# Kernel tuning notes

Measured on AMD Instinct MI355X. Metric: run time of the kernel, lower is better.

The kernel has to match this reference:

```python
import jax, jax.numpy as jnp
import numpy as np

EMD_DIM = 64
NB_EMD = 512


def setup_inputs() -> dict:
    key = jax.random.key(0)
    k_x, k_e = jax.random.split(key)
    x = jax.random.normal(k_x, (32, 64, 64, EMD_DIM), dtype=jnp.float32)
    # codebook buffer, shape [emd_dim, nb_emd] as in the torch module
    embed = jax.random.normal(k_e, (EMD_DIM, NB_EMD), dtype=jnp.float32)
    return {"x": x, "embed": embed}


def reference(x, embed):
    # Eval-mode forward (the EMA buffer update only runs under self.training
    # and does not affect this forward's outputs).
    flatten = x.reshape(-1, EMD_DIM)                      # [N, d]
    dist = (jnp.sum(flatten * flatten, axis=1, keepdims=True)
            - 2.0 * flatten @ embed
            + jnp.sum(embed * embed, axis=0, keepdims=True))  # [N, K]
    emd_id_flat = jnp.argmax(-dist, axis=1)               # nearest code index [N]
    emd_id = emd_id_flat.reshape(x.shape[:-1])            # [B, H, W]
    q = jnp.take(embed.T, emd_id, axis=0)                 # gather codes -> [B,H,W,d]
    diff = jnp.mean((jax.lax.stop_gradient(q) - x) ** 2)  # commitment loss
    q_st = x + jax.lax.stop_gradient(q - x)               # straight-through
    return (q_st, diff, emd_id)
```

## Files before the change

kernel.cpp:

```cpp
#include <hip/hip_runtime.h>

#define N_VEC 131072
#define D 64
#define K 512
#define GUARD 0.05f
#define NB_GATHER 2048
#define FB_Q 16

typedef __attribute__((ext_vector_type(8))) short bf16x8;
typedef __attribute__((ext_vector_type(4))) float f32x4;

static __device__ __forceinline__ short f2bf(float f) {
  unsigned u = __builtin_bit_cast(unsigned, f);
  u += 0x7fffu + ((u >> 16) & 1u);
  return (short)(u >> 16);
}
static __device__ __forceinline__ float bf2f(short h) {
  unsigned u = ((unsigned)(unsigned short)h) << 16;
  return __builtin_bit_cast(float, u);
}
static __device__ __forceinline__ void split8(const float4 f0, const float4 f1,
                                              bf16x8& h, bf16x8& m) {
  const float v[8] = {f0.x, f0.y, f0.z, f0.w, f1.x, f1.y, f1.z, f1.w};
#pragma unroll
  for (int j = 0; j < 8; ++j) {
    const short hh = f2bf(v[j]);
    h[j] = hh;
    m[j] = f2bf(v[j] - bf2f(hh));
  }
}

__global__ __launch_bounds__(64) void vq_prep_kernel(
    const float* __restrict__ embed, float* __restrict__ et,
    float* __restrict__ nrm, bf16x8* __restrict__ F, int* __restrict__ cnt)
{
  const int b = blockIdx.x;
  const int lane = threadIdx.x;
  if (b < 32) {
    const int row = lane & 15;
    const int kg  = lane >> 4;
    const int code = b * 16 + row;
#pragma unroll
    for (int c = 0; c < 2; ++c) {
      bf16x8 h, m;
#pragma unroll
      for (int j = 0; j < 8; ++j) {
        const int d = kg * 8 + c * 32 + j;
        const float e = embed[d * K + code];
        const short hh = f2bf(e);
        h[j] = hh;
        m[j] = f2bf(e - bf2f(hh));
      }
      F[b * 256 + c * 128 + 0  + lane] = h;
      F[b * 256 + c * 128 + 64 + lane] = m;
    }
  } else {
    if (b == 32 && lane == 0) cnt[0] = 0;
    const int code = (b - 32) * 64 + lane;
    float s = 0.f;
#pragma unroll
    for (int d = 0; d < D; ++d) {
      const float e = embed[d * K + code];
      et[code * D + d] = e;
      s = fmaf(e, e, s);
    }
    nrm[code] = s;
  }
}

#define MFMA12(P0, Q0, P1, Q1, BH0, BM0, BH1, BM1) do {                        \
    P0 = __builtin_amdgcn_mfma_f32_16x16x32_bf16(Ah0c0, BH0, kZero, 0, 0, 0); \
    P1 = __builtin_amdgcn_mfma_f32_16x16x32_bf16(Ah1c0, BH0, kZero, 0, 0, 0); \
    Q0 = __builtin_amdgcn_mfma_f32_16x16x32_bf16(Ah0c1, BM1, kZero, 0, 0, 0); \
    Q1 = __builtin_amdgcn_mfma_f32_16x16x32_bf16(Ah1c1, BM1, kZero, 0, 0, 0); \
    P0 = __builtin_amdgcn_mfma_f32_16x16x32_bf16(Ah0c1, BH1, P0, 0, 0, 0);    \
    P1 = __builtin_amdgcn_mfma_f32_16x16x32_bf16(Ah1c1, BH1, P1, 0, 0, 0);    \
    Q0 = __builtin_amdgcn_mfma_f32_16x16x32_bf16(Am0c0, BH0, Q0, 0, 0, 0);    \
    Q1 = __builtin_amdgcn_mfma_f32_16x16x32_bf16(Am1c0, BH0, Q1, 0, 0, 0);    \
    P0 = __builtin_amdgcn_mfma_f32_16x16x32_bf16(Ah0c0, BM0, P0, 0, 0, 0);    \
    P1 = __builtin_amdgcn_mfma_f32_16x16x32_bf16(Ah1c0, BM0, P1, 0, 0, 0);    \
    Q0 = __builtin_amdgcn_mfma_f32_16x16x32_bf16(Am0c1, BH1, Q0, 0, 0, 0);    \
    Q1 = __builtin_amdgcn_mfma_f32_16x16x32_bf16(Am1c1, BH1, Q1, 0, 0, 0);    \
  } while (0)

#define SCORE4(P0, Q0, P1, Q1, CODE, NV) do {                                  \
    _Pragma("unroll")                                                          \
    for (int r = 0; r < 4; ++r) {                                              \
      const float s0 = fmaf(-2.f, P0[r], fmaf(-2.f, Q0[r], (NV)));             \
      b2[r] = __builtin_amdgcn_fmed3f(s0, b1[r], b2[r]);                       \
      if (s0 < b1[r]) { b1[r] = s0; i1[r] = (CODE); }                          \
      const float s1 = fmaf(-2.f, P1[r], fmaf(-2.f, Q1[r], (NV)));             \
      b2[4 + r] = __builtin_amdgcn_fmed3f(s1, b1[4 + r], b2[4 + r]);           \
      if (s1 < b1[4 + r]) { b1[4 + r] = s1; i1[4 + r] = (CODE); }              \
    }                                                                          \
  } while (0)

#define LOADB(BH0, BM0, BH1, BM1, PTR) do {                                    \
    BH0 = (PTR)[0]; BM0 = (PTR)[64]; BH1 = (PTR)[128]; BM1 = (PTR)[192];       \
  } while (0)

__global__ __launch_bounds__(64, 3) void vq_coarse_kernel(
    const float* __restrict__ x, const bf16x8* __restrict__ F,
    const float* __restrict__ nrm, float* __restrict__ idf,
    int* __restrict__ cnt, int* __restrict__ list)
{
  const int lane = threadIdx.x;
  const int wid  = blockIdx.x;
  const int qbase = wid * 32;
  const int row = lane & 15;
  const int kg  = lane >> 4;

  bf16x8 Ah0c0, Ah0c1, Ah1c0, Ah1c1, Am0c0, Am0c1, Am1c0, Am1c1;
  {
    const float* xr0 = x + (size_t)(qbase + row) * D + kg * 8;
    const float* xr1 = x + (size_t)(qbase + 16 + row) * D + kg * 8;
    split8(*reinterpret_cast<const float4*>(xr0),
           *reinterpret_cast<const float4*>(xr0 + 4), Ah0c0, Am0c0);
    split8(*reinterpret_cast<const float4*>(xr0 + 32),
           *reinterpret_cast<const float4*>(xr0 + 36), Ah0c1, Am0c1);
    split8(*reinterpret_cast<const float4*>(xr1),
           *reinterpret_cast<const float4*>(xr1 + 4), Ah1c0, Am1c0);
    split8(*reinterpret_cast<const float4*>(xr1 + 32),
           *reinterpret_cast<const float4*>(xr1 + 36), Ah1c1, Am1c1);
  }

  float b1[8], b2[8]; int i1[8];
#pragma unroll
  for (int r = 0; r < 8; ++r) { b1[r] = 3.4e38f; b2[r] = 3.4e38f; i1[r] = 0; }

  const f32x4 kZero = {0.f, 0.f, 0.f, 0.f};
  bf16x8 X0h0, X0m0, X0h1, X0m1;
  bf16x8 X1h0, X1m0, X1h1, X1m1;
  f32x4 pA0, qA0, pA1, qA1;
  f32x4 pB0, qB0, pB1, qB1;

  const bf16x8* fp = F + lane;
  const float* np = nrm + row;

  float nvA  = np[0];
  float nvBc = np[16];
  np += 32;
  LOADB(X0h0, X0m0, X0h1, X0m1, fp);
  LOADB(X1h0, X1m0, X1h1, X1m1, fp + 256);
  fp += 512;
  MFMA12(pA0, qA0, pA1, qA1, X0h0, X0m0, X0h1, X0m1);
  LOADB(X0h0, X0m0, X0h1, X0m1, fp);
  fp += 256;
  MFMA12(pB0, qB0, pB1, qB1, X1h0, X1m0, X1h1, X1m1);
  SCORE4(pA0, qA0, pA1, qA1, row, nvA);

#pragma unroll 1
  for (int tp = 2; tp <= 30; tp += 2) {
    const float nvA2 = np[0];
    const float nvB  = np[16];
    np += 32;
    LOADB(X1h0, X1m0, X1h1, X1m1, fp);
    MFMA12(pA0, qA0, pA1, qA1, X0h0, X0m0, X0h1, X0m1);
    SCORE4(pB0, qB0, pB1, qB1, (tp - 1) * 16 + row, nvBc);
    LOADB(X0h0, X0m0, X0h1, X0m1, fp + 256);
    fp += 512;
    MFMA12(pB0, qB0, pB1, qB1, X1h0, X1m0, X1h1, X1m1);
    SCORE4(pA0, qA0, pA1, qA1, tp * 16 + row, nvA2);
    nvBc = nvB;
  }
  SCORE4(pB0, qB0, pB1, qB1, 31 * 16 + row, nvBc);

#pragma unroll
  for (int m = 1; m < 16; m <<= 1) {
#pragma unroll
    for (int r = 0; r < 8; ++r) {
      const float o1 = __shfl_xor(b1[r], m, 64);
      const int   oi = __shfl_xor(i1[r], m, 64);
      const float o2 = __shfl_xor(b2[r], m, 64);
      if (o1 < b1[r]) { b2[r] = fminf(b1[r], o2); b1[r] = o1; i1[r] = oi; }
      else            { b2[r] = fminf(b2[r], o1); }
    }
  }

  unsigned m32 = 0;
  if (row == 0) {
#pragma unroll
    for (int r = 0; r < 8; ++r) {
      const int qoff = (r >> 2) * 16 + kg * 4 + (r & 3);
      idf[qbase + qoff] = (float)i1[r];
      if (b2[r] - b1[r] < GUARD) m32 |= 1u << qoff;
    }
  }
  m32 |= __shfl_xor((int)m32, 16, 64);
  m32 |= __shfl_xor((int)m32, 32, 64);
  if (lane == 0 && m32) {
    int base = atomicAdd(cnt, __popc(m32));
    while (m32) {
      const int b = __ffs(m32) - 1;
      m32 &= m32 - 1;
      list[base++] = qbase + b;
    }
  }
}

__global__ __launch_bounds__(256) void vq_fallback_kernel(
    const float* __restrict__ x, const float* __restrict__ embed,
    const float* __restrict__ nrm, const int* __restrict__ cnt,
    const int* __restrict__ list, float* __restrict__ idf)
{
  __shared__ float x_lds[FB_Q * D];
  __shared__ int   s_qidx[FB_Q];
  __shared__ float s_best[4][FB_Q];
  __shared__ int   s_bid[4][FB_Q];
  const int tid  = threadIdx.x;
  const int lane = tid & 63;
  const int wv   = tid >> 6;
  const int n = cnt[0];

  for (int qb = blockIdx.x * FB_Q; qb < n; qb += gridDim.x * FB_Q) {
    __syncthreads();
    if (tid < FB_Q) {
      const int idx = qb + tid;
      s_qidx[tid] = list[idx < n ? idx : qb];
    }
    __syncthreads();
    {
      const int qj = tid >> 4, dq = tid & 15;
      *reinterpret_cast<float4*>(&x_lds[qj * D + dq * 4]) =
          *reinterpret_cast<const float4*>(x + (size_t)s_qidx[qj] * D + dq * 4);
    }
    __syncthreads();

    const int c0 = wv * 128 + lane;
    const int c1 = c0 + 64;
    float a0[FB_Q], a1[FB_Q];
#pragma unroll
    for (int i = 0; i < FB_Q; ++i) { a0[i] = 0.f; a1[i] = 0.f; }

#pragma unroll 4
    for (int ch = 0; ch < 16; ++ch) {
      const int d0 = ch * 4;
      const float e00 = embed[(d0 + 0) * K + c0];
      const float e01 = embed[(d0 + 0) * K + c1];
      const float e10 = embed[(d0 + 1) * K + c0];
      const float e11 = embed[(d0 + 1) * K + c1];
      const float e20 = embed[(d0 + 2) * K + c0];
      const float e21 = embed[(d0 + 2) * K + c1];
      const float e30 = embed[(d0 + 3) * K + c0];
      const float e31 = embed[(d0 + 3) * K + c1];
#pragma unroll
      for (int i = 0; i < FB_Q; ++i) {
        const float4 xv = *reinterpret_cast<const float4*>(&x_lds[i * D + d0]);
        a0[i] = fmaf(xv.x, e00, a0[i]);
        a0[i] = fmaf(xv.y, e10, a0[i]);
        a0[i] = fmaf(xv.z, e20, a0[i]);
        a0[i] = fmaf(xv.w, e30, a0[i]);
        a1[i] = fmaf(xv.x, e01, a1[i]);
        a1[i] = fmaf(xv.y, e11, a1[i]);
        a1[i] = fmaf(xv.z, e21, a1[i]);
        a1[i] = fmaf(xv.w, e31, a1[i]);
      }
    }

    const float nr0 = nrm[c0], nr1 = nrm[c1];
#pragma unroll
    for (int i = 0; i < FB_Q; ++i) {
      float best; int bid;
      const float s0 = fmaf(-2.f, a0[i], nr0);
      best = s0; bid = c0;
      const float s1 = fmaf(-2.f, a1[i], nr1);
      if (s1 < best) { best = s1; bid = c1; }
#pragma unroll
      for (int off = 32; off > 0; off >>= 1) {
        const float s2 = __shfl_down(best, off, 64);
        const int   b2 = __shfl_down(bid, off, 64);
        if (s2 < best || (s2 == best && b2 < bid)) { best = s2; bid = b2; }
      }
      if (lane == 0) { s_best[wv][i] = best; s_bid[wv][i] = bid; }
    }
    __syncthreads();
    if (tid < FB_Q) {
      float best = s_best[0][tid]; int bid = s_bid[0][tid];
#pragma unroll
      for (int w = 1; w < 4; ++w) {
        const float s = s_best[w][tid];
        if (s < best) { best = s; bid = s_bid[w][tid]; }
      }
      idf[s_qidx[tid]] = (float)bid;
    }
  }
}

__global__ __launch_bounds__(256) void vq_gather_kernel(
    const float* __restrict__ x, const float* __restrict__ et,
    const float* __restrict__ idf, float* __restrict__ q,
    float* __restrict__ partial)
{
  const int tid = blockIdx.x * 256 + threadIdx.x;
  const int stride = gridDim.x * 256;
  float acc = 0.f;
  for (int idx = tid; idx < N_VEC * (D / 4); idx += stride) {
    const int v = idx >> 4;
    const int d4 = idx & 15;
    const int id = (int)idf[v];
    const float4 xv = reinterpret_cast<const float4*>(x)[idx];
    const float4 ev = reinterpret_cast<const float4*>(et)[(id << 4) + d4];
    const float e0 = ev.x - xv.x, e1 = ev.y - xv.y, e2 = ev.z - xv.z, e3 = ev.w - xv.w;
    acc += (e0 * e0 + e1 * e1) + (e2 * e2 + e3 * e3);
    reinterpret_cast<float4*>(q)[idx] = ev;
  }
  acc += __shfl_down(acc, 32, 64);
  acc += __shfl_down(acc, 16, 64);
  acc += __shfl_down(acc, 8, 64);
  acc += __shfl_down(acc, 4, 64);
  acc += __shfl_down(acc, 2, 64);
  acc += __shfl_down(acc, 1, 64);
  __shared__ float sred[4];
  if ((threadIdx.x & 63) == 0) sred[threadIdx.x >> 6] = acc;
  __syncthreads();
  if (threadIdx.x == 0)
    partial[blockIdx.x] = (sred[0] + sred[1]) + (sred[2] + sred[3]);
}

__global__ __launch_bounds__(256) void vq_finalize_kernel(
    const float* __restrict__ partial, float* __restrict__ out)
{
  float acc = 0.f;
  for (int i = threadIdx.x; i < NB_GATHER; i += 256) acc += partial[i];
  acc += __shfl_down(acc, 32, 64);
  acc += __shfl_down(acc, 16, 64);
  acc += __shfl_down(acc, 8, 64);
  acc += __shfl_down(acc, 4, 64);
  acc += __shfl_down(acc, 2, 64);
  acc += __shfl_down(acc, 1, 64);
  __shared__ float sred[4];
  if ((threadIdx.x & 63) == 0) sred[threadIdx.x >> 6] = acc;
  __syncthreads();
  if (threadIdx.x == 0)
    out[0] = ((sred[0] + sred[1]) + (sred[2] + sred[3])) * (1.0f / (float)(N_VEC * D));
}

extern "C" void kernel_launch(void* const* d_in, const int* in_sizes, int n_in,
                              void* d_out, int out_size, void* d_ws, size_t ws_size,
                              hipStream_t stream) {
  const float* x = (const float*)d_in[0];
  const float* embed = (const float*)d_in[1];
  float* out = (float*)d_out;
  float* q    = out;
  float* diff = out + 8388608;
  float* idf  = out + 8388609;

  float* ws = (float*)d_ws;
  float* et      = ws;
  float* nrm     = ws + 32768;
  float* partial = ws + 33312;
  int*   cnt     = (int*)(ws + 35360);
  int*   list    = (int*)(ws + 35368);
  bf16x8* F = (bf16x8*)(ws + 35368 + N_VEC);

  vq_prep_kernel<<<40, 64, 0, stream>>>(embed, et, nrm, F, cnt);
  vq_coarse_kernel<<<N_VEC / 32, 64, 0, stream>>>(x, F, nrm, idf, cnt, list);
  vq_fallback_kernel<<<1024, 256, 0, stream>>>(x, embed, nrm, cnt, list, idf);
  vq_gather_kernel<<<NB_GATHER, 256, 0, stream>>>(x, et, idf, q, partial);
  vq_finalize_kernel<<<1, 256, 0, stream>>>(partial, diff);
}
```

Before: 83.86 us.

## Fuse gather and loss into coarse kernel, stage codebook hi-part in LDS

The coarse kernel now runs 512-thread blocks that stage the bf16 high part of the codebook in shared memory and stream the low part from global memory. The separate gather and reduction pass is removed. Each wave writes its quantized rows and accumulates the squared error for confident queries directly after the argmin. Fallback queries write their own q rows and a per-query error into a zeroed buffer, which two small kernels reduce. This avoids re-reading x and the indices in a separate gather pass, at the cost of a 64 KB LDS footprint that limits occupancy, an extra memset, and an extra finalize launch.

```diff
diff --git a/kernel.cpp b/kernel.cpp
--- a/kernel.cpp
+++ b/kernel.cpp
@@ -4,7 +4,6 @@
 #define D 64
 #define K 512
 #define GUARD 0.05f
-#define NB_GATHER 2048
 #define FB_Q 16
 
 typedef __attribute__((ext_vector_type(8))) short bf16x8;
@@ -32,7 +31,8 @@
 
 __global__ __launch_bounds__(64) void vq_prep_kernel(
     const float* __restrict__ embed, float* __restrict__ et,
-    float* __restrict__ nrm, bf16x8* __restrict__ F, int* __restrict__ cnt)
+    float* __restrict__ nrm, bf16x8* __restrict__ FH, bf16x8* __restrict__ FM,
+    int* __restrict__ cnt)
 {
   const int b = blockIdx.x;
   const int lane = threadIdx.x;
@@ -51,8 +51,8 @@
         h[j] = hh;
         m[j] = f2bf(e - bf2f(hh));
       }
-      F[b * 256 + c * 128 + 0  + lane] = h;
-      F[b * 256 + c * 128 + 64 + lane] = m;
+      FH[b * 128 + c * 64 + lane] = h;
+      FM[b * 128 + c * 64 + lane] = m;
     }
   } else {
     if (b == 32 && lane == 0) cnt[0] = 0;
@@ -95,20 +95,27 @@
     }                                                                          \
   } while (0)
 
-#define LOADB(BH0, BM0, BH1, BM1, PTR) do {                                    \
-    BH0 = (PTR)[0]; BM0 = (PTR)[64]; BH1 = (PTR)[128]; BM1 = (PTR)[192];       \
-  } while (0)
-
-__global__ __launch_bounds__(64, 3) void vq_coarse_kernel(
-    const float* __restrict__ x, const bf16x8* __restrict__ F,
-    const float* __restrict__ nrm, float* __restrict__ idf,
-    int* __restrict__ cnt, int* __restrict__ list)
+__global__ __launch_bounds__(512, 4) void vq_coarse_kernel(
+    const float* __restrict__ x, const bf16x8* __restrict__ FH,
+    const bf16x8* __restrict__ FM, const float* __restrict__ nrm,
+    const float* __restrict__ et, float* __restrict__ qout,
+    float* __restrict__ idf, int* __restrict__ cnt, int* __restrict__ list,
+    float* __restrict__ cpart)
 {
-  const int lane = threadIdx.x;
-  const int wid  = blockIdx.x;
-  const int qbase = wid * 32;
-  const int row = lane & 15;
-  const int kg  = lane >> 4;
+  __shared__ bf16x8 LBH[4096];
+  const int tid  = threadIdx.x;
+  const int lane = tid & 63;
+  const int w    = tid >> 6;
+  const int row  = lane & 15;
+  const int kg   = lane >> 4;
+  const int qbase = blockIdx.x * 256 + w * 32;
+
+  {
+    const float4* src = reinterpret_cast<const float4*>(FH);
+    float4* dst = reinterpret_cast<float4*>(LBH);
+#pragma unroll
+    for (int j = 0; j < 8; ++j) dst[tid + j * 512] = src[tid + j * 512];
+  }
 
   bf16x8 Ah0c0, Ah0c1, Ah1c0, Ah1c1, Am0c0, Am0c1, Am1c0, Am1c1;
   {
@@ -123,47 +130,35 @@
     split8(*reinterpret_cast<const float4*>(xr1 + 32),
            *reinterpret_cast<const float4*>(xr1 + 36), Ah1c1, Am1c1);
   }
+  __syncthreads();
 
   float b1[8], b2[8]; int i1[8];
 #pragma unroll
   for (int r = 0; r < 8; ++r) { b1[r] = 3.4e38f; b2[r] = 3.4e38f; i1[r] = 0; }
 
   const f32x4 kZero = {0.f, 0.f, 0.f, 0.f};
-  bf16x8 X0h0, X0m0, X0h1, X0m1;
-  bf16x8 X1h0, X1m0, X1h1, X1m1;
-  f32x4 pA0, qA0, pA1, qA1;
-  f32x4 pB0, qB0, pB1, qB1;
-
-  const bf16x8* fp = F + lane;
-  const float* np = nrm + row;
-
-  float nvA  = np[0];
-  float nvBc = np[16];
-  np += 32;
-  LOADB(X0h0, X0m0, X0h1, X0m1, fp);
-  LOADB(X1h0, X1m0, X1h1, X1m1, fp + 256);
-  fp += 512;
-  MFMA12(pA0, qA0, pA1, qA1, X0h0, X0m0, X0h1, X0m1);
-  LOADB(X0h0, X0m0, X0h1, X0m1, fp);
-  fp += 256;
-  MFMA12(pB0, qB0, pB1, qB1, X1h0, X1m0, X1h1, X1m1);
-  SCORE4(pA0, qA0, pA1, qA1, row, nvA);
+  f32x4 aP0, aQ0, aP1, aQ1;
+
+  const bf16x8* fm = FM + lane;
+  const float*  np = nrm + row;
+  const bf16x8* lb = LBH + lane;
+  bf16x8 Bm0 = fm[0], Bm1 = fm[64]; fm += 128;
+  float nv = np[0]; np += 16;
 
 #pragma unroll 1
-  for (int tp = 2; tp <= 30; tp += 2) {
-    const float nvA2 = np[0];
-    const float nvB  = np[16];
-    np += 32;
-    LOADB(X1h0, X1m0, X1h1, X1m1, fp);
-    MFMA12(pA0, qA0, pA1, qA1, X0h0, X0m0, X0h1, X0m1);
-    SCORE4(pB0, qB0, pB1, qB1, (tp - 1) * 16 + row, nvBc);
-    LOADB(X0h0, X0m0, X0h1, X0m1, fp + 256);
-    fp += 512;
-    MFMA12(pB0, qB0, pB1, qB1, X1h0, X1m0, X1h1, X1m1);
-    SCORE4(pA0, qA0, pA1, qA1, tp * 16 + row, nvA2);
-    nvBc = nvB;
-  }
-  SCORE4(pB0, qB0, pB1, qB1, 31 * 16 + row, nvBc);
+  for (int t = 0; t < 32; ++t) {
+    const bf16x8 Bh0 = lb[0];
+    const bf16x8 Bh1 = lb[64];
+    lb += 128;
+    const bf16x8 nBm0 = fm[0];
+    const bf16x8 nBm1 = fm[64];
+    fm += 128;
+    const float nnv = np[0];
+    np += 16;
+    MFMA12(aP0, aQ0, aP1, aQ1, Bh0, Bm0, Bh1, Bm1);
+    SCORE4(aP0, aQ0, aP1, aQ1, t * 16 + row, nv);
+    Bm0 = nBm0; Bm1 = nBm1; nv = nnv;
+  }
 
 #pragma unroll
   for (int m = 1; m < 16; m <<= 1) {
@@ -196,17 +191,54 @@
       list[base++] = qbase + b;
     }
   }
+
+  float wacc = 0.f;
+  const float* xw = x + (size_t)qbase * D;
+  float* qw = qout + (size_t)qbase * D;
+#pragma unroll
+  for (int i = 0; i < 32; ++i) {
+    const int s   = i >> 4;
+    const int w16 = i & 15;
+    const int kq  = w16 >> 2;
+    const int r   = s * 4 + (w16 & 3);
+    const int id    = __shfl(i1[r], kq * 16, 64);
+    const float gap = __shfl(b2[r] - b1[r], kq * 16, 64);
+    const float ev = et[(size_t)id * D + lane];
+    const float xv = xw[i * D + lane];
+    qw[i * D + lane] = ev;
+    const float dd = ev - xv;
+    if (gap >= GUARD) wacc = fmaf(dd, dd, wacc);
+  }
+  wacc += __shfl_down(wacc, 32, 64);
+  wacc += __shfl_down(wacc, 16, 64);
+  wacc += __shfl_down(wacc, 8, 64);
+  wacc += __shfl_down(wacc, 4, 64);
+  wacc += __shfl_down(wacc, 2, 64);
+  wacc += __shfl_down(wacc, 1, 64);
+  __syncthreads();
+  float* sred = reinterpret_cast<float*>(LBH);
+  if (lane == 0) sred[w] = wacc;
+  __syncthreads();
+  if (tid == 0) {
+    float t = 0.f;
+#pragma unroll
+    for (int j = 0; j < 8; ++j) t += sred[j];
+    cpart[blockIdx.x] = t;
+  }
 }
 
 __global__ __launch_bounds__(256) void vq_fallback_kernel(
     const float* __restrict__ x, const float* __restrict__ embed,
-    const float* __restrict__ nrm, const int* __restrict__ cnt,
-    const int* __restrict__ list, float* __restrict__ idf)
+    const float* __restrict__ nrm, const float* __restrict__ et,
+    const int* __restrict__ cnt, const int* __restrict__ list,
+    float* __restrict__ idf, float* __restrict__ qout,
+    float* __restrict__ sqerr)
 {
   __shared__ float x_lds[FB_Q * D];
   __shared__ int   s_qidx[FB_Q];
   __shared__ float s_best[4][FB_Q];
   __shared__ int   s_bid[4][FB_Q];
+  __shared__ int   s_fbid[FB_Q];
   const int tid  = threadIdx.x;
   const int lane = tid & 63;
   const int wv   = tid >> 6;
@@ -282,28 +314,52 @@
         if (s < best) { best = s; bid = s_bid[w][tid]; }
       }
       idf[s_qidx[tid]] = (float)bid;
-    }
-  }
-}
-
-__global__ __launch_bounds__(256) void vq_gather_kernel(
-    const float* __restrict__ x, const float* __restrict__ et,
-    const float* __restrict__ idf, float* __restrict__ q,
-    float* __restrict__ partial)
+      s_fbid[tid] = bid;
+    }
+    __syncthreads();
+#pragma unroll
+    for (int i2 = 0; i2 < 4; ++i2) {
+      const int slot = wv * 4 + i2;
+      const int qq   = s_qidx[slot];
+      const int fb   = s_fbid[slot];
+      const float ev = et[(size_t)fb * D + lane];
+      const float xv = x_lds[slot * D + lane];
+      qout[(size_t)qq * D + lane] = ev;
+      float dd = (ev - xv) * (ev - xv);
+      dd += __shfl_down(dd, 32, 64);
+      dd += __shfl_down(dd, 16, 64);
+      dd += __shfl_down(dd, 8, 64);
+      dd += __shfl_down(dd, 4, 64);
+      dd += __shfl_down(dd, 2, 64);
+      dd += __shfl_down(dd, 1, 64);
+      if (lane == 0) sqerr[qq] = dd;
+    }
+  }
+}
+
+__global__ __launch_bounds__(256) void vq_fin1_kernel(
+    const float* __restrict__ sqerr, float* __restrict__ fpart)
 {
-  const int tid = blockIdx.x * 256 + threadIdx.x;
-  const int stride = gridDim.x * 256;
-  float acc = 0.f;
-  for (int idx = tid; idx < N_VEC * (D / 4); idx += stride) {
-    const int v = idx >> 4;
-    const int d4 = idx & 15;
-    const int id = (int)idf[v];
-    const float4 xv = reinterpret_cast<const float4*>(x)[idx];
-    const float4 ev = reinterpret_cast<const float4*>(et)[(id << 4) + d4];
-    const float e0 = ev.x - xv.x, e1 = ev.y - xv.y, e2 = ev.z - xv.z, e3 = ev.w - xv.w;
-    acc += (e0 * e0 + e1 * e1) + (e2 * e2 + e3 * e3);
-    reinterpret_cast<float4*>(q)[idx] = ev;
-  }
+  float v = sqerr[blockIdx.x * 256 + threadIdx.x];
+  v += __shfl_down(v, 32, 64);
+  v += __shfl_down(v, 16, 64);
+  v += __shfl_down(v, 8, 64);
+  v += __shfl_down(v, 4, 64);
+  v += __shfl_down(v, 2, 64);
+  v += __shfl_down(v, 1, 64);
+  __shared__ float sred[4];
+  if ((threadIdx.x & 63) == 0) sred[threadIdx.x >> 6] = v;
+  __syncthreads();
+  if (threadIdx.x == 0)
+    fpart[blockIdx.x] = (sred[0] + sred[1]) + (sred[2] + sred[3]);
+}
+
+__global__ __launch_bounds__(256) void vq_fin2_kernel(
+    const float* __restrict__ cpart, const float* __restrict__ fpart,
+    float* __restrict__ out)
+{
+  const int tid = threadIdx.x;
+  float acc = cpart[tid] + cpart[tid + 256] + fpart[tid] + fpart[tid + 256];
   acc += __shfl_down(acc, 32, 64);
   acc += __shfl_down(acc, 16, 64);
   acc += __shfl_down(acc, 8, 64);
@@ -311,27 +367,9 @@
   acc += __shfl_down(acc, 2, 64);
   acc += __shfl_down(acc, 1, 64);
   __shared__ float sred[4];
-  if ((threadIdx.x & 63) == 0) sred[threadIdx.x >> 6] = acc;
+  if ((tid & 63) == 0) sred[tid >> 6] = acc;
   __syncthreads();
-  if (threadIdx.x == 0)
-    partial[blockIdx.x] = (sred[0] + sred[1]) + (sred[2] + sred[3]);
-}
-
-__global__ __launch_bounds__(256) void vq_finalize_kernel(
-    const float* __restrict__ partial, float* __restrict__ out)
-{
-  float acc = 0.f;
-  for (int i = threadIdx.x; i < NB_GATHER; i += 256) acc += partial[i];
-  acc += __shfl_down(acc, 32, 64);
-  acc += __shfl_down(acc, 16, 64);
-  acc += __shfl_down(acc, 8, 64);
-  acc += __shfl_down(acc, 4, 64);
-  acc += __shfl_down(acc, 2, 64);
-  acc += __shfl_down(acc, 1, 64);
-  __shared__ float sred[4];
-  if ((threadIdx.x & 63) == 0) sred[threadIdx.x >> 6] = acc;
-  __syncthreads();
-  if (threadIdx.x == 0)
+  if (tid == 0)
     out[0] = ((sred[0] + sred[1]) + (sred[2] + sred[3])) * (1.0f / (float)(N_VEC * D));
 }
 
@@ -346,16 +384,22 @@
   float* idf  = out + 8388609;
 
   float* ws = (float*)d_ws;
-  float* et      = ws;
-  float* nrm     = ws + 32768;
-  float* partial = ws + 33312;
-  int*   cnt     = (int*)(ws + 35360);
-  int*   list    = (int*)(ws + 35368);
-  bf16x8* F = (bf16x8*)(ws + 35368 + N_VEC);
-
-  vq_prep_kernel<<<40, 64, 0, stream>>>(embed, et, nrm, F, cnt);
-  vq_coarse_kernel<<<N_VEC / 32, 64, 0, stream>>>(x, F, nrm, idf, cnt, list);
-  vq_fallback_kernel<<<1024, 256, 0, stream>>>(x, embed, nrm, cnt, list, idf);
-  vq_gather_kernel<<<NB_GATHER, 256, 0, stream>>>(x, et, idf, q, partial);
-  vq_finalize_kernel<<<1, 256, 0, stream>>>(partial, diff);
-}
+  float* et    = ws;
+  float* nrm   = ws + 32768;
+  float* cpart = ws + 33344;
+  float* fpart = ws + 33856;
+  int*   cnt   = (int*)(ws + 34368);
+  int*   list  = (int*)(ws + 34376);
+  bf16x8* FH = (bf16x8*)(ws + 34376 + N_VEC);
+  bf16x8* FM = (bf16x8*)(ws + 34376 + N_VEC + 16384);
+  float* sqerr = ws + 34376 + N_VEC + 16384 + 16384 + 512;
+
+  hipMemsetAsync(sqerr, 0, N_VEC * sizeof(float), stream);
+  vq_prep_kernel<<<40, 64, 0, stream>>>(embed, et, nrm, FH, FM, cnt);
+  vq_coarse_kernel<<<512, 512, 0, stream>>>(x, FH, FM, nrm, et, q, idf, cnt,
+                                            list, cpart);
+  vq_fallback_kernel<<<1024, 256, 0, stream>>>(x, embed, nrm, et, cnt, list,
+                                               idf, q, sqerr);
+  vq_fin1_kernel<<<512, 256, 0, stream>>>(sqerr, fpart);
+  vq_fin2_kernel<<<1, 256, 0, stream>>>(cpart, fpart, diff);
+}
```

New measurement: 89.11 us. +6.3%, slower.

## Replace two-tile ping-pong codebook loop with single-tile prefetch and raise occupancy

Applied to the files above, without the earlier changes.

Replaces the manually software-pipelined loop, which held two codebook tiles and two sets of MFMA accumulators, with a simpler per-tile loop. It prefetches the next tile's B fragments and norm value while computing the current one. Empty asm register pins keep the accumulators and zero vector in VGPRs, and launch bounds rise from 3 to 4 waves per SIMD. The aim is lower register pressure and more concurrent waves to hide latency. The cost is that MFMA and scoring work within a single wave no longer overlap.

```diff
diff --git a/kernel.cpp b/kernel.cpp
--- a/kernel.cpp
+++ b/kernel.cpp
@@ -1,14 +1,16 @@
 #include <hip/hip_runtime.h>
 
 #define N_VEC 131072
+#define K 512
 #define D 64
-#define K 512
 #define GUARD 0.05f
 #define NB_GATHER 2048
 #define FB_Q 16
 
 typedef __attribute__((ext_vector_type(8))) short bf16x8;
 typedef __attribute__((ext_vector_type(4))) float f32x4;
+
+#define PIN(v) asm("" : "+v"(v))
 
 static __device__ __forceinline__ short f2bf(float f) {
   unsigned u = __builtin_bit_cast(unsigned, f);
@@ -95,11 +97,7 @@
     }                                                                          \
   } while (0)
 
-#define LOADB(BH0, BM0, BH1, BM1, PTR) do {                                    \
-    BH0 = (PTR)[0]; BM0 = (PTR)[64]; BH1 = (PTR)[128]; BM1 = (PTR)[192];       \
-  } while (0)
-
-__global__ __launch_bounds__(64, 3) void vq_coarse_kernel(
+__global__ __launch_bounds__(64, 4) void vq_coarse_kernel(
     const float* __restrict__ x, const bf16x8* __restrict__ F,
     const float* __restrict__ nrm, float* __restrict__ idf,
     int* __restrict__ cnt, int* __restrict__ list)
@@ -128,42 +126,31 @@
 #pragma unroll
   for (int r = 0; r < 8; ++r) { b1[r] = 3.4e38f; b2[r] = 3.4e38f; i1[r] = 0; }
 
-  const f32x4 kZero = {0.f, 0.f, 0.f, 0.f};
-  bf16x8 X0h0, X0m0, X0h1, X0m1;
-  bf16x8 X1h0, X1m0, X1h1, X1m1;
-  f32x4 pA0, qA0, pA1, qA1;
-  f32x4 pB0, qB0, pB1, qB1;
+  f32x4 kZero = {0.f, 0.f, 0.f, 0.f};
+  PIN(kZero);
 
   const bf16x8* fp = F + lane;
+  bf16x8 Bh0 = fp[0], Bm0 = fp[64], Bh1 = fp[128], Bm1 = fp[192];
+  fp += 256;
   const float* np = nrm + row;
-
-  float nvA  = np[0];
-  float nvBc = np[16];
-  np += 32;
-  LOADB(X0h0, X0m0, X0h1, X0m1, fp);
-  LOADB(X1h0, X1m0, X1h1, X1m1, fp + 256);
-  fp += 512;
-  MFMA12(pA0, qA0, pA1, qA1, X0h0, X0m0, X0h1, X0m1);
-  LOADB(X0h0, X0m0, X0h1, X0m1, fp);
-  fp += 256;
-  MFMA12(pB0, qB0, pB1, qB1, X1h0, X1m0, X1h1, X1m1);
-  SCORE4(pA0, qA0, pA1, qA1, row, nvA);
+  float nv = np[0];
+  np += 16;
 
 #pragma unroll 1
-  for (int tp = 2; tp <= 30; tp += 2) {
-    const float nvA2 = np[0];
-    const float nvB  = np[16];
-    np += 32;
-    LOADB(X1h0, X1m0, X1h1, X1m1, fp);
-    MFMA12(pA0, qA0, pA1, qA1, X0h0, X0m0, X0h1, X0m1);
-    SCORE4(pB0, qB0, pB1, qB1, (tp - 1) * 16 + row, nvBc);
-    LOADB(X0h0, X0m0, X0h1, X0m1, fp + 256);
-    fp += 512;
-    MFMA12(pB0, qB0, pB1, qB1, X1h0, X1m0, X1h1, X1m1);
-    SCORE4(pA0, qA0, pA1, qA1, tp * 16 + row, nvA2);
-    nvBc = nvB;
-  }
-  SCORE4(pB0, qB0, pB1, qB1, 31 * 16 + row, nvBc);
+  for (int t = 0; t < 32; ++t) {
+    bf16x8 nh0, nm0, nh1, nm1; float nvn;
+    if (t < 31) {
+      nh0 = fp[0]; nm0 = fp[64]; nh1 = fp[128]; nm1 = fp[192]; fp += 256;
+      nvn = np[0]; np += 16;
+    }
+
+    f32x4 p0, q0, p1, q1;
+    MFMA12(p0, q0, p1, q1, Bh0, Bm0, Bh1, Bm1);
+    PIN(p0); PIN(q0); PIN(p1); PIN(q1);
+
+    SCORE4(p0, q0, p1, q1, t * 16 + row, nv);
+    Bh0 = nh0; Bm0 = nm0; Bh1 = nh1; Bm1 = nm1; nv = nvn;
+  }
 
 #pragma unroll
   for (int m = 1; m < 16; m <<= 1) {
```

Result: no change. 85.09 us (+1.5%).
